# Kernel optimization log

Hardware: AMD Instinct MI355X
Metric: run time of the kernel (lower is better)

Reference implementation:

```python
import jax, jax.numpy as jnp
import numpy as np

EPS = 1e-6


def setup_inputs() -> dict:
    key = jax.random.key(0)
    kx, kw = jax.random.split(key)
    B, C, N = 8, 256, 2048
    x = jax.random.normal(kx, (B, C, N), dtype=jnp.float32)
    # nn.Linear(dim*2, 2, bias=False): weight shape [2, 2*C]
    W = jax.random.normal(kw, (2, 2 * C), dtype=jnp.float32) * (1.0 / np.sqrt(2 * C))
    return {"x": x, "W": W}


def reference(x, W):
    B, C, N = x.shape
    # cosine similarity matrix [B, N, N]
    sim = jnp.einsum('bcn,bcm->bnm', x, x)
    # torch: sqrt(sum(x^2 + 1e-6, dim=1)) -> eps added per-channel before sum
    norms = jnp.sqrt(jnp.sum(x * x + EPS, axis=1))            # [B, N]
    io_abs = sim / (norms[:, :, None] * norms[:, None, :])    # [B, N, N]
    # zero the diagonal (fill_diagonal_(0)) before argmax
    io_abs = io_abs * (1.0 - jnp.eye(N, dtype=io_abs.dtype))
    idx = jnp.argmax(io_abs, axis=2)                          # [B, N] nearest-neighbor per token
    # gather retrieved features: f_re[b, :, n] = x[b, :, idx[b, n]]
    f_re = jnp.take_along_axis(x, idx[:, None, :], axis=2)    # [B, C, N]
    # gated fusion
    fus = jnp.concatenate([x, f_re], axis=1).transpose(0, 2, 1)  # [B, N, 2C]
    w = jax.nn.softmax(fus @ W.T, axis=-1)                    # [B, N, 2]
    w = w.transpose(0, 2, 1)                                  # [B, 2, N]
    out = x * w[:, 0:1, :] + f_re * w[:, 1:2, :]
    return (out, f_re)
```

## Files before the change

kernel.cpp:

```cpp
#include <hip/hip_runtime.h>
#include <hip/hip_bf16.h>
#include <math.h>

constexpr int B_ = 8;
constexpr int C_ = 256;
constexpr int N_ = 2048;
constexpr int CN_ = C_ * N_;
constexpr int TOT_ = B_ * C_ * N_;
constexpr int NTILES = 16;
constexpr int NPAIRS = 136;

typedef __attribute__((ext_vector_type(8))) short bf16x8;
typedef __attribute__((ext_vector_type(4))) float f32x4;

__device__ __forceinline__ void g2l16(const void* g, void* l) {
    __builtin_amdgcn_global_load_lds(
        (const __attribute__((address_space(1))) void*)g,
        (__attribute__((address_space(3))) void*)l, 16, 0, 0);
}

__device__ __forceinline__ unsigned short bits(__hip_bfloat16 h) {
    union { __hip_bfloat16 b; unsigned short u; } cv;
    cv.b = h;
    return cv.u;
}

__device__ __forceinline__ float b2f(short s) {
    union { float f; unsigned u; } cv;
    cv.u = ((unsigned)(unsigned short)s) << 16;
    return cv.f;
}

__global__ __launch_bounds__(256) void convert_kernel(const float* __restrict__ x,
                                                      __hip_bfloat16* __restrict__ hiT,
                                                      __hip_bfloat16* __restrict__ loT,
                                                      float* __restrict__ normacc) {
    const int blk = blockIdx.x;
    const int batch = blk & 7;
    const int nt = (blk >> 3) & 31;
    const int ctile = blk >> 8;
    const int n0 = nt << 6, c0 = ctile << 6;
    const int t = threadIdx.x;
    const int i = t & 63, j = t >> 6;

    __shared__ float tb[64][65];
    __shared__ float red[4][64];

    float s = 0.f;
    const float* xp = x + (size_t)batch * CN_ + (size_t)c0 * N_ + n0 + i;
#pragma unroll 4
    for (int r = 0; r < 16; ++r) {
        const int cl = j + r * 4;
        const float v = xp[(size_t)cl * N_];
        tb[cl][i] = v;
        s += v * v;
    }
    red[j][i] = s;
    __syncthreads();

    const int cp = t & 31;
    const int c2 = cp << 1;
    const int nb = t >> 5;
#pragma unroll 4
    for (int r = 0; r < 8; ++r) {
        const int n = nb + r * 8;
        const float v0 = tb[c2][n], v1 = tb[c2 + 1][n];
        const size_t o = ((size_t)batch * N_ + n0 + n) * C_ + c0 + c2;
        const __hip_bfloat16 h0 = __float2bfloat16(v0);
        const __hip_bfloat16 h1 = __float2bfloat16(v1);
        const __hip_bfloat16 g0 = __float2bfloat16(v0 - __bfloat162float(h0));
        const __hip_bfloat16 g1 = __float2bfloat16(v1 - __bfloat162float(h1));
        ((unsigned*)hiT)[o >> 1] = ((unsigned)bits(h1) << 16) | bits(h0);
        ((unsigned*)loT)[o >> 1] = ((unsigned)bits(g1) << 16) | bits(g0);
    }
    if (j == 0) {
        const float tt = red[0][i] + red[1][i] + red[2][i] + red[3][i];
        atomicAdd(normacc + batch * N_ + n0 + i, tt);
    }
}

__global__ void rnorm_fin_kernel(const float* __restrict__ normacc,
                                 float* __restrict__ rnorm) {
    const int t = blockIdx.x * 256 + threadIdx.x;
    rnorm[t] = 1.0f / sqrtf(normacc[t] + 256.0f * 1e-6f);
}

__global__ __launch_bounds__(256) void gram_mfma_kernel(
        const __hip_bfloat16* __restrict__ hiT, const __hip_bfloat16* __restrict__ loT,
        const float* __restrict__ rnorm,
        float* __restrict__ pval, int* __restrict__ pidx, float* __restrict__ pval2) {
    const int blk = blockIdx.x;
    const int batch = blk & 7;
    int p = blk >> 3;
    int bn = 0;
    while (p >= NTILES - bn) { p -= NTILES - bn; ++bn; }
    const int bm = bn + p;
    const bool diag = (bn == bm);
    const int n0 = bn << 7, m0 = bm << 7;

    __shared__ short As[128 * 64];
    __shared__ short Bs[128 * 64];
    float (*rv1)[2] = (float(*)[2])(As + 0);
    int (*ri1)[2] = (int(*)[2])(As + 512);
    float (*rv2)[2] = (float(*)[2])(As + 1024);
    float (*cv1)[2] = (float(*)[2])(As + 1536);
    int (*ci1)[2] = (int(*)[2])(As + 2048);
    float (*cv2)[2] = (float(*)[2])(As + 2560);
    float* rnA = (float*)(As + 3072);

    const int tid = threadIdx.x;
    const int l = tid & 63, w = tid >> 6;
    const int lm = l & 15, q = l >> 4;
    const int wn = (w >> 1) << 6, wm = (w & 1) << 6;

    f32x4 acc[4][4];
#pragma unroll
    for (int rt = 0; rt < 4; ++rt)
#pragma unroll
        for (int ct = 0; ct < 4; ++ct) acc[rt][ct] = (f32x4){0.f, 0.f, 0.f, 0.f};

    const size_t bbase = (size_t)batch * CN_;

    for (int seg = 0; seg < 3; ++seg) {
        const __hip_bfloat16* Asrc = (seg == 2) ? loT : hiT;
        const __hip_bfloat16* Bsrc = (seg == 1) ? loT : hiT;
        for (int kt = 0; kt < 4; ++kt) {
            const int kb = kt << 6;
            __syncthreads();
#pragma unroll
            for (int pp = 0; pp < 4; ++pp) {
                const int slot = tid + pp * 256;
                const int r = slot >> 3, sidx = slot & 7;
                const int sw = sidx ^ (r & 7);
                g2l16(Asrc + bbase + (size_t)(n0 + r) * C_ + kb + sw * 8, As + slot * 8);
                g2l16(Bsrc + bbase + (size_t)(m0 + r) * C_ + kb + sw * 8, Bs + slot * 8);
            }
            __syncthreads();
#pragma unroll
            for (int kq = 0; kq < 2; ++kq) {
                bf16x8 af[4], bfr[4];
#pragma unroll
                for (int rt = 0; rt < 4; ++rt) {
                    const int row = wn + rt * 16 + lm;
                    af[rt] = *(const bf16x8*)(As + row * 64 + (((kq << 2) | q) ^ (lm & 7)) * 8);
                }
#pragma unroll
                for (int ct = 0; ct < 4; ++ct) {
                    const int row = wm + ct * 16 + lm;
                    bfr[ct] = *(const bf16x8*)(Bs + row * 64 + (((kq << 2) | q) ^ (lm & 7)) * 8);
                }
#pragma unroll
                for (int rt = 0; rt < 4; ++rt)
#pragma unroll
                    for (int ct = 0; ct < 4; ++ct)
                        acc[rt][ct] = __builtin_amdgcn_mfma_f32_16x16x32_bf16(
                            af[rt], bfr[ct], acc[rt][ct], 0, 0, 0);
            }
        }
    }

    __syncthreads();
    if (tid < 128) rnA[tid] = rnorm[batch * N_ + n0 + tid];

    float rnm[4];
#pragma unroll
    for (int ct = 0; ct < 4; ++ct) rnm[ct] = rnorm[batch * N_ + m0 + wm + ct * 16 + lm];

#pragma unroll
    for (int rt = 0; rt < 4; ++rt) {
#pragma unroll
        for (int r = 0; r < 4; ++r) {
            const int nrow = n0 + wn + rt * 16 + q * 4 + r;
            float v1 = -3.4e38f, v2 = -3.4e38f;
            int i1 = 0x7fffffff;
#pragma unroll
            for (int ct = 0; ct < 4; ++ct) {
                const int m = m0 + wm + ct * 16 + lm;
                const float v = acc[rt][ct][r] * rnm[ct];
                if (m == nrow) continue;
                if (v > v1) { v2 = v1; v1 = v; i1 = m; }
                else if (v > v2) v2 = v;
            }
#pragma unroll
            for (int d = 1; d < 16; d <<= 1) {
                const float ov1 = __shfl_xor(v1, d, 64);
                const int oi1 = __shfl_xor(i1, d, 64);
                const float ov2 = __shfl_xor(v2, d, 64);
                if (ov1 > v1 || (ov1 == v1 && oi1 < i1)) {
                    v2 = fmaxf(v1, ov2); v1 = ov1; i1 = oi1;
                } else {
                    v2 = fmaxf(v2, ov1);
                }
            }
            if (lm == 0) {
                const int rloc = wn + rt * 16 + q * 4 + r;
                rv1[rloc][w & 1] = v1;
                ri1[rloc][w & 1] = i1;
                rv2[rloc][w & 1] = v2;
            }
        }
    }
    __syncthreads();

    if (!diag) {
        float rnn[4][4];
#pragma unroll
        for (int rt = 0; rt < 4; ++rt)
#pragma unroll
            for (int r = 0; r < 4; ++r) rnn[rt][r] = rnA[wn + rt * 16 + q * 4 + r];
#pragma unroll
        for (int ct = 0; ct < 4; ++ct) {
            float v1 = -3.4e38f, v2 = -3.4e38f;
            int i1 = 0x7fffffff;
#pragma unroll
            for (int rt = 0; rt < 4; ++rt) {
#pragma unroll
                for (int r = 0; r < 4; ++r) {
                    const float v = acc[rt][ct][r] * rnn[rt][r];
                    const int nn = n0 + wn + rt * 16 + q * 4 + r;
                    if (v > v1) { v2 = v1; v1 = v; i1 = nn; }
                    else if (v > v2) v2 = v;
                }
            }
#pragma unroll
            for (int d = 16; d < 64; d <<= 1) {
                const float ov1 = __shfl_xor(v1, d, 64);
                const int oi1 = __shfl_xor(i1, d, 64);
                const float ov2 = __shfl_xor(v2, d, 64);
                if (ov1 > v1 || (ov1 == v1 && oi1 < i1)) {
                    v2 = fmaxf(v1, ov2); v1 = ov1; i1 = oi1;
                } else {
                    v2 = fmaxf(v2, ov1);
                }
            }
            if (q == 0) {
                const int mloc = wm + ct * 16 + lm;
                cv1[mloc][w >> 1] = v1;
                ci1[mloc][w >> 1] = i1;
                cv2[mloc][w >> 1] = v2;
            }
        }
    }
    __syncthreads();

    if (tid < 128) {
        {
            float v1 = rv1[tid][0]; int i1 = ri1[tid][0]; float v2 = rv2[tid][0];
            const float ov1 = rv1[tid][1]; const int oi1 = ri1[tid][1]; const float ov2 = rv2[tid][1];
            if (ov1 > v1 || (ov1 == v1 && oi1 < i1)) { v2 = fmaxf(v1, ov2); v1 = ov1; i1 = oi1; }
            else v2 = fmaxf(v2, ov1);
            const size_t gi = (size_t)(batch * NTILES + bm) * N_ + n0 + tid;
            pval[gi] = v1; pidx[gi] = i1; pval2[gi] = v2;
        }
        if (!diag) {
            float v1 = cv1[tid][0]; int i1 = ci1[tid][0]; float v2 = cv2[tid][0];
            const float ov1 = cv1[tid][1]; const int oi1 = ci1[tid][1]; const float ov2 = cv2[tid][1];
            if (ov1 > v1 || (ov1 == v1 && oi1 < i1)) { v2 = fmaxf(v1, ov2); v1 = ov1; i1 = oi1; }
            else v2 = fmaxf(v2, ov1);
            const size_t gi = (size_t)(batch * NTILES + bn) * N_ + m0 + tid;
            pval[gi] = v1; pidx[gi] = i1; pval2[gi] = v2;
        }
    }
}

__global__ void combine_kernel(const float* __restrict__ pval, const int* __restrict__ pidx,
                               const float* __restrict__ pval2, int* __restrict__ fidx,
                               int* __restrict__ rcnt, int* __restrict__ ridx) {
    const int t = blockIdx.x * 256 + threadIdx.x;
    const int batch = t >> 11, n = t & 2047;
    float v1 = -3.4e38f, v2 = -3.4e38f;
    int i1 = 0x7fffffff;
    for (int s = 0; s < NTILES; ++s) {
        const size_t gi = (size_t)(batch * NTILES + s) * N_ + n;
        const float ov1 = pval[gi]; const int oi1 = pidx[gi]; const float ov2 = pval2[gi];
        if (ov1 > v1 || (ov1 == v1 && oi1 < i1)) { v2 = fmaxf(v1, ov2); v1 = ov1; i1 = oi1; }
        else v2 = fmaxf(v2, ov1);
    }
    fidx[t] = i1;
    if (v1 - v2 < 1e-4f) {
        const int slot = atomicAdd(rcnt, 1);
        ridx[slot] = t;
    }
}

__global__ __launch_bounds__(256) void rescue_kernel(const float* __restrict__ x,
                                                     const float* __restrict__ rnorm,
                                                     const int* __restrict__ rcnt,
                                                     const int* __restrict__ ridx,
                                                     int* __restrict__ fidx) {
    const int cnt = *rcnt;
    const int tid = threadIdx.x;
    __shared__ float bv[256];
    __shared__ int bi[256];
    for (int rr = blockIdx.x; rr < cnt; rr += gridDim.x) {
        const int t = ridx[rr];
        const int batch = t >> 11, n = t & 2047;
        const float* xb = x + (size_t)batch * CN_;
        float s[8];
#pragma unroll
        for (int k = 0; k < 8; ++k) s[k] = 0.f;
        for (int c = 0; c < C_; ++c) {
            const float xc = xb[(size_t)c * N_ + n];
            const float* xr = xb + (size_t)c * N_;
#pragma unroll
            for (int k = 0; k < 8; ++k) s[k] += xc * xr[tid + (k << 8)];
        }
        float best = -3.4e38f;
        int besti = 0x7fffffff;
#pragma unroll
        for (int k = 0; k < 8; ++k) {
            const int m = tid + (k << 8);
            const float v = s[k] * rnorm[batch * N_ + m];
            if (m != n && v > best) { best = v; besti = m; }
        }
        bv[tid] = best; bi[tid] = besti;
        __syncthreads();
        for (int sft = 128; sft > 0; sft >>= 1) {
            if (tid < sft) {
                const float ov = bv[tid + sft]; const int oi = bi[tid + sft];
                if (ov > bv[tid] || (ov == bv[tid] && oi < bi[tid])) { bv[tid] = ov; bi[tid] = oi; }
            }
            __syncthreads();
        }
        if (tid == 0) fidx[t] = bi[0];
        __syncthreads();
    }
}

__global__ __launch_bounds__(256) void finish_kernel(const float* __restrict__ x,
                                                     const __hip_bfloat16* __restrict__ hiT,
                                                     const __hip_bfloat16* __restrict__ loT,
                                                     const float* __restrict__ W,
                                                     const int* __restrict__ fidx,
                                                     float* __restrict__ out) {
    const int batch = blockIdx.x & 7;
    const int nt = blockIdx.x >> 3;
    const int n0 = nt << 4;
    const int t = threadIdx.x;
    const int i = t & 15, cg = t >> 4;

    __shared__ float Wl[1024];
    __shared__ int il[16];
    __shared__ float l0r[16][17], l1r[16][17];
    __shared__ float w0s[16], w1s[16];

    for (int u = t; u < 1024; u += 256) Wl[u] = W[u];
    if (t < 16) il[t] = fidx[batch * N_ + n0 + t];
    __syncthreads();

    const float* xb = x + (size_t)batch * CN_ + n0 + i;
    const int myidx = il[i];
    const size_t row = ((size_t)batch * N_ + myidx) * C_ + cg * 16;

    float fvv[16];
    {
        const bf16x8* hp = (const bf16x8*)(hiT + row);
        const bf16x8* lp = (const bf16x8*)(loT + row);
#pragma unroll
        for (int v8 = 0; v8 < 2; ++v8) {
            const bf16x8 h = hp[v8];
            const bf16x8 g = lp[v8];
#pragma unroll
            for (int e = 0; e < 8; ++e) fvv[v8 * 8 + e] = b2f(h[e]) + b2f(g[e]);
        }
    }

    float l0 = 0.f, l1 = 0.f;
#pragma unroll
    for (int cc = 0; cc < 16; ++cc) {
        const int c = cg * 16 + cc;
        const float xv = xb[(size_t)c * N_];
        l0 += xv * Wl[c] + fvv[cc] * Wl[256 + c];
        l1 += xv * Wl[512 + c] + fvv[cc] * Wl[768 + c];
    }
    l0r[cg][i] = l0;
    l1r[cg][i] = l1;
    __syncthreads();
    if (t < 16) {
        float L0 = 0.f, L1 = 0.f;
#pragma unroll
        for (int g = 0; g < 16; ++g) { L0 += l0r[g][t]; L1 += l1r[g][t]; }
        const float mx = fmaxf(L0, L1);
        const float e0 = expf(L0 - mx);
        const float e1 = expf(L1 - mx);
        const float inv = 1.0f / (e0 + e1);
        w0s[t] = e0 * inv;
        w1s[t] = e1 * inv;
    }
    __syncthreads();
    const float w0 = w0s[i], w1 = w1s[i];

#pragma unroll
    for (int cc = 0; cc < 16; ++cc) {
        const int c = cg * 16 + cc;
        const size_t off = (size_t)batch * CN_ + (size_t)c * N_ + n0 + i;
        const float xv = xb[(size_t)c * N_];
        out[off] = xv * w0 + fvv[cc] * w1;
        out[TOT_ + off] = fvv[cc];
    }
}

extern "C" void kernel_launch(void* const* d_in, const int* in_sizes, int n_in,
                              void* d_out, int out_size, void* d_ws, size_t ws_size,
                              hipStream_t stream) {
    const float* x = (const float*)d_in[0];
    const float* W = (const float*)d_in[1];
    float* out = (float*)d_out;

    const size_t BF_BYTES = (size_t)TOT_ * 2;
    const size_t NORM_BYTES = (size_t)B_ * N_ * 4;
    const size_t P_BYTES = (size_t)B_ * NTILES * N_ * 4;

    uint8_t* p = (uint8_t*)d_ws;
    __hip_bfloat16* hiT = (__hip_bfloat16*)p; p += BF_BYTES;
    __hip_bfloat16* loT = (__hip_bfloat16*)p; p += BF_BYTES;
    float* rnorm = (float*)p; p += NORM_BYTES;
    float* normacc = (float*)p; p += NORM_BYTES;
    float* pval = (float*)p; p += P_BYTES;
    int* pidx = (int*)p; p += P_BYTES;
    float* pval2 = (float*)p; p += P_BYTES;
    int* fidx = (int*)p; p += NORM_BYTES;
    int* rcnt = (int*)p; p += 256;
    int* ridx = (int*)p; p += NORM_BYTES;

    hipMemsetAsync(rcnt, 0, 4, stream);
    hipMemsetAsync(normacc, 0, NORM_BYTES, stream);
    convert_kernel<<<1024, 256, 0, stream>>>(x, hiT, loT, normacc);
    rnorm_fin_kernel<<<64, 256, 0, stream>>>(normacc, rnorm);
    gram_mfma_kernel<<<B_ * NPAIRS, 256, 0, stream>>>(hiT, loT, rnorm, pval, pidx, pval2);
    combine_kernel<<<64, 256, 0, stream>>>(pval, pidx, pval2, fidx, rcnt, ridx);
    rescue_kernel<<<64, 256, 0, stream>>>(x, rnorm, rcnt, ridx, fidx);
    finish_kernel<<<1024, 256, 0, stream>>>(x, hiT, loT, W, fidx, out);
}
```

Before: 207.3 us.

## Load Gram MFMA fragments directly from global with register double buffering

The Gram kernel stops staging tiles through LDS with global_load_lds and barriers. Each lane now loads its bf16x8 fragments straight from global memory into registers, with a double-buffered prefetch over 24 unrolled k-steps and launch bounds set to 3 blocks per SM. The separate rnorm finalize kernel is removed: reciprocal norms are computed inline from normacc in the Gram and rescue kernels, and the two memsets are merged into one. This removes LDS traffic, barriers and one launch, but gives up LDS reuse, so global and L2 traffic rises and register pressure grows.

```diff
diff --git a/kernel.cpp b/kernel.cpp
--- a/kernel.cpp
+++ b/kernel.cpp
@@ -9,15 +9,10 @@
 constexpr int TOT_ = B_ * C_ * N_;
 constexpr int NTILES = 16;
 constexpr int NPAIRS = 136;
+constexpr float EPS_SUM = 256.0f * 1e-6f;
 
 typedef __attribute__((ext_vector_type(8))) short bf16x8;
 typedef __attribute__((ext_vector_type(4))) float f32x4;
-
-__device__ __forceinline__ void g2l16(const void* g, void* l) {
-    __builtin_amdgcn_global_load_lds(
-        (const __attribute__((address_space(1))) void*)g,
-        (__attribute__((address_space(3))) void*)l, 16, 0, 0);
-}
 
 __device__ __forceinline__ unsigned short bits(__hip_bfloat16 h) {
     union { __hip_bfloat16 b; unsigned short u; } cv;
@@ -79,15 +74,9 @@
     }
 }
 
-__global__ void rnorm_fin_kernel(const float* __restrict__ normacc,
-                                 float* __restrict__ rnorm) {
-    const int t = blockIdx.x * 256 + threadIdx.x;
-    rnorm[t] = 1.0f / sqrtf(normacc[t] + 256.0f * 1e-6f);
-}
-
-__global__ __launch_bounds__(256) void gram_mfma_kernel(
+__global__ __launch_bounds__(256, 3) void gram_mfma_kernel(
         const __hip_bfloat16* __restrict__ hiT, const __hip_bfloat16* __restrict__ loT,
-        const float* __restrict__ rnorm,
+        const float* __restrict__ normacc,
         float* __restrict__ pval, int* __restrict__ pidx, float* __restrict__ pval2) {
     const int blk = blockIdx.x;
     const int batch = blk & 7;
@@ -98,15 +87,13 @@
     const bool diag = (bn == bm);
     const int n0 = bn << 7, m0 = bm << 7;
 
-    __shared__ short As[128 * 64];
-    __shared__ short Bs[128 * 64];
-    float (*rv1)[2] = (float(*)[2])(As + 0);
-    int (*ri1)[2] = (int(*)[2])(As + 512);
-    float (*rv2)[2] = (float(*)[2])(As + 1024);
-    float (*cv1)[2] = (float(*)[2])(As + 1536);
-    int (*ci1)[2] = (int(*)[2])(As + 2048);
-    float (*cv2)[2] = (float(*)[2])(As + 2560);
-    float* rnA = (float*)(As + 3072);
+    __shared__ float rv1[128][2];
+    __shared__ int ri1[128][2];
+    __shared__ float rv2[128][2];
+    __shared__ float cv1[128][2];
+    __shared__ int ci1[128][2];
+    __shared__ float cv2[128][2];
+    __shared__ float rnA[128];
 
     const int tid = threadIdx.x;
     const int l = tid & 63, w = tid >> 6;
@@ -120,51 +107,58 @@
         for (int ct = 0; ct < 4; ++ct) acc[rt][ct] = (f32x4){0.f, 0.f, 0.f, 0.f};
 
     const size_t bbase = (size_t)batch * CN_;
-
-    for (int seg = 0; seg < 3; ++seg) {
-        const __hip_bfloat16* Asrc = (seg == 2) ? loT : hiT;
-        const __hip_bfloat16* Bsrc = (seg == 1) ? loT : hiT;
-        for (int kt = 0; kt < 4; ++kt) {
-            const int kb = kt << 6;
-            __syncthreads();
-#pragma unroll
-            for (int pp = 0; pp < 4; ++pp) {
-                const int slot = tid + pp * 256;
-                const int r = slot >> 3, sidx = slot & 7;
-                const int sw = sidx ^ (r & 7);
-                g2l16(Asrc + bbase + (size_t)(n0 + r) * C_ + kb + sw * 8, As + slot * 8);
-                g2l16(Bsrc + bbase + (size_t)(m0 + r) * C_ + kb + sw * 8, Bs + slot * 8);
-            }
-            __syncthreads();
-#pragma unroll
-            for (int kq = 0; kq < 2; ++kq) {
-                bf16x8 af[4], bfr[4];
-#pragma unroll
-                for (int rt = 0; rt < 4; ++rt) {
-                    const int row = wn + rt * 16 + lm;
-                    af[rt] = *(const bf16x8*)(As + row * 64 + (((kq << 2) | q) ^ (lm & 7)) * 8);
-                }
-#pragma unroll
-                for (int ct = 0; ct < 4; ++ct) {
-                    const int row = wm + ct * 16 + lm;
-                    bfr[ct] = *(const bf16x8*)(Bs + row * 64 + (((kq << 2) | q) ^ (lm & 7)) * 8);
-                }
-#pragma unroll
-                for (int rt = 0; rt < 4; ++rt)
-#pragma unroll
-                    for (int ct = 0; ct < 4; ++ct)
-                        acc[rt][ct] = __builtin_amdgcn_mfma_f32_16x16x32_bf16(
-                            af[rt], bfr[ct], acc[rt][ct], 0, 0, 0);
-            }
-        }
-    }
-
-    __syncthreads();
-    if (tid < 128) rnA[tid] = rnorm[batch * N_ + n0 + tid];
+    const size_t rowA = bbase + (size_t)(n0 + wn + lm) * C_ + q * 8;
+    const size_t rowB = bbase + (size_t)(m0 + wm + lm) * C_ + q * 8;
+
+    const short* const hs = (const short*)hiT;
+    const short* const ls = (const short*)loT;
+
+    bf16x8 a0[4], b0[4], a1[4], b1[4];
+
+#define GRAM_LD(S, AF, BF)                                                  \
+    {                                                                       \
+        constexpr int seg_ = (S) >> 3, kt_ = (S) & 7;                       \
+        const short* ap_ = ((seg_ == 2) ? ls : hs) + rowA + kt_ * 32;       \
+        const short* bp_ = ((seg_ == 1) ? ls : hs) + rowB + kt_ * 32;       \
+        _Pragma("unroll") for (int t_ = 0; t_ < 4; ++t_) {                  \
+            AF[t_] = *(const bf16x8*)(ap_ + t_ * 16 * C_);                  \
+            BF[t_] = *(const bf16x8*)(bp_ + t_ * 16 * C_);                  \
+        }                                                                   \
+    }
+
+    GRAM_LD(0, a0, b0);
+#pragma unroll
+    for (int s = 0; s < 24; ++s) {
+        bf16x8* ac = (s & 1) ? a1 : a0;
+        bf16x8* bc = (s & 1) ? b1 : b0;
+        bf16x8* an = (s & 1) ? a0 : a1;
+        bf16x8* bn_ = (s & 1) ? b0 : b1;
+        if (s + 1 < 24) {
+            switch (s + 1) {
+#define CASE_LD(SS) case SS: GRAM_LD(SS, an, bn_); break;
+                CASE_LD(1) CASE_LD(2) CASE_LD(3) CASE_LD(4) CASE_LD(5)
+                CASE_LD(6) CASE_LD(7) CASE_LD(8) CASE_LD(9) CASE_LD(10)
+                CASE_LD(11) CASE_LD(12) CASE_LD(13) CASE_LD(14) CASE_LD(15)
+                CASE_LD(16) CASE_LD(17) CASE_LD(18) CASE_LD(19) CASE_LD(20)
+                CASE_LD(21) CASE_LD(22) CASE_LD(23)
+#undef CASE_LD
+            }
+        }
+#pragma unroll
+        for (int rt = 0; rt < 4; ++rt)
+#pragma unroll
+            for (int ct = 0; ct < 4; ++ct)
+                acc[rt][ct] = __builtin_amdgcn_mfma_f32_16x16x32_bf16(
+                    ac[rt], bc[ct], acc[rt][ct], 0, 0, 0);
+    }
+#undef GRAM_LD
+
+    if (tid < 128) rnA[tid] = 1.0f / sqrtf(normacc[batch * N_ + n0 + tid] + EPS_SUM);
 
     float rnm[4];
 #pragma unroll
-    for (int ct = 0; ct < 4; ++ct) rnm[ct] = rnorm[batch * N_ + m0 + wm + ct * 16 + lm];
+    for (int ct = 0; ct < 4; ++ct)
+        rnm[ct] = 1.0f / sqrtf(normacc[batch * N_ + m0 + wm + ct * 16 + lm] + EPS_SUM);
 
 #pragma unroll
     for (int rt = 0; rt < 4; ++rt) {
@@ -284,7 +278,7 @@
 }
 
 __global__ __launch_bounds__(256) void rescue_kernel(const float* __restrict__ x,
-                                                     const float* __restrict__ rnorm,
+                                                     const float* __restrict__ normacc,
                                                      const int* __restrict__ rcnt,
                                                      const int* __restrict__ ridx,
                                                      int* __restrict__ fidx) {
@@ -310,7 +304,7 @@
 #pragma unroll
         for (int k = 0; k < 8; ++k) {
             const int m = tid + (k << 8);
-            const float v = s[k] * rnorm[batch * N_ + m];
+            const float v = s[k] / sqrtf(normacc[batch * N_ + m] + EPS_SUM);
             if (m != n && v > best) { best = v; besti = m; }
         }
         bv[tid] = best; bi[tid] = besti;
@@ -414,21 +408,18 @@
     uint8_t* p = (uint8_t*)d_ws;
     __hip_bfloat16* hiT = (__hip_bfloat16*)p; p += BF_BYTES;
     __hip_bfloat16* loT = (__hip_bfloat16*)p; p += BF_BYTES;
-    float* rnorm = (float*)p; p += NORM_BYTES;
     float* normacc = (float*)p; p += NORM_BYTES;
+    int* rcnt = (int*)p; p += 256;
     float* pval = (float*)p; p += P_BYTES;
     int* pidx = (int*)p; p += P_BYTES;
     float* pval2 = (float*)p; p += P_BYTES;
     int* fidx = (int*)p; p += NORM_BYTES;
-    int* rcnt = (int*)p; p += 256;
     int* ridx = (int*)p; p += NORM_BYTES;
 
-    hipMemsetAsync(rcnt, 0, 4, stream);
-    hipMemsetAsync(normacc, 0, NORM_BYTES, stream);
+    hipMemsetAsync(normacc, 0, NORM_BYTES + 256, stream);
     convert_kernel<<<1024, 256, 0, stream>>>(x, hiT, loT, normacc);
-    rnorm_fin_kernel<<<64, 256, 0, stream>>>(normacc, rnorm);
-    gram_mfma_kernel<<<B_ * NPAIRS, 256, 0, stream>>>(hiT, loT, rnorm, pval, pidx, pval2);
+    gram_mfma_kernel<<<B_ * NPAIRS, 256, 0, stream>>>(hiT, loT, normacc, pval, pidx, pval2);
     combine_kernel<<<64, 256, 0, stream>>>(pval, pidx, pval2, fidx, rcnt, ridx);
-    rescue_kernel<<<64, 256, 0, stream>>>(x, rnorm, rcnt, ridx, fidx);
+    rescue_kernel<<<64, 256, 0, stream>>>(x, normacc, rcnt, ridx, fidx);
     finish_kernel<<<1024, 256, 0, stream>>>(x, hiT, loT, W, fidx, out);
 }
```

Result: slower. 353.1 us (+70.3%).
